# Kernel optimization log

Hardware: AMD Instinct MI355X
Metric: run time of the kernel (lower is better)

The kernel has to match this reference:

```python
import jax, jax.numpy as jnp
import numpy as np

B, T, I, Hd = 64, 1024, 256, 256
SIGMA = 0.01


def setup_inputs() -> dict:
    key = jax.random.key(0)
    ks = jax.random.split(key, 7)
    return {
        "inputs": jax.random.normal(ks[0], (B, T, I), dtype=jnp.float32),
        "W_xz": jax.random.normal(ks[1], (I, Hd), dtype=jnp.float32) * SIGMA,
        "W_hz": jax.random.normal(ks[2], (Hd, Hd), dtype=jnp.float32) * SIGMA,
        "b_z": jnp.zeros((Hd,), dtype=jnp.float32),
        "W_xr": jax.random.normal(ks[3], (I, Hd), dtype=jnp.float32) * SIGMA,
        "W_hr": jax.random.normal(ks[4], (Hd, Hd), dtype=jnp.float32) * SIGMA,
        "b_r": jnp.zeros((Hd,), dtype=jnp.float32),
        "W_xh": jax.random.normal(ks[5], (I, Hd), dtype=jnp.float32) * SIGMA,
        "W_hh": jax.random.normal(ks[6], (Hd, Hd), dtype=jnp.float32) * SIGMA,
        "b_h": jnp.zeros((Hd,), dtype=jnp.float32),
    }


def reference(inputs, W_xz, W_hz, b_z, W_xr, W_hr, b_r, W_xh, W_hh, b_h):
    # inputs: [B, T, I] -> time-major [T, B, I]
    xs = jnp.swapaxes(inputs, 0, 1)
    # Precompute all input-side projections in three big GEMMs (same math,
    # hoisted out of the recurrence): [T, B, Hd] each.
    xz = jnp.einsum("tbi,ih->tbh", xs, W_xz) + b_z
    xr = jnp.einsum("tbi,ih->tbh", xs, W_xr) + b_r
    xh = jnp.einsum("tbi,ih->tbh", xs, W_xh) + b_h

    H0 = jnp.zeros((inputs.shape[0], W_hz.shape[0]), dtype=inputs.dtype)

    def step(H, x):
        xz_t, xr_t, xh_t = x
        Z = jax.nn.sigmoid(xz_t + H @ W_hz)
        R = jax.nn.sigmoid(xr_t + H @ W_hr)
        H_tilde = jnp.tanh(xh_t + (R * H) @ W_hh)
        H_new = Z * H + (1.0 - Z) * H_tilde
        return H_new, H_new

    H_last, outs = jax.lax.scan(step, H0, (xz, xr, xh))
    # outputs stacked along dim=1: [B, T, Hd]
    outputs = jnp.swapaxes(outs, 0, 1)
    return outputs, H_last
```

## Files before the change

### kernel.cpp

```cpp
#include <hip/hip_runtime.h>
#include <math.h>

#define BB 64
#define TT 1024
#define II 256
#define HD 256

typedef unsigned short ushort_t;
typedef unsigned int uint_t;

typedef short sh8 __attribute__((ext_vector_type(8)));
typedef float fx4 __attribute__((ext_vector_type(4)));

__device__ __forceinline__ ushort_t f2bf(float f) {
    uint_t u = __float_as_uint(f);
    uint_t r = (u + 0x7fffu + ((u >> 16) & 1u)) >> 16;
    return (ushort_t)r;
}
__device__ __forceinline__ float bf2f(ushort_t v) {
    return __uint_as_float(((uint_t)v) << 16);
}

__device__ __forceinline__ float fast_rcp(float x) {
#if __has_builtin(__builtin_amdgcn_rcpf)
    return __builtin_amdgcn_rcpf(x);
#else
    return 1.f / x;
#endif
}
__device__ __forceinline__ float sigm(float x) {
    return fast_rcp(1.f + __expf(-x));
}
__device__ __forceinline__ float tanh_fast(float x) {
    return 1.f - 2.f * fast_rcp(1.f + __expf(2.f * x));
}

__device__ __forceinline__ fx4 mfma16(sh8 a, sh8 b, fx4 c) {
    return __builtin_amdgcn_mfma_f32_16x16x32_bf16(a, b, c, 0, 0, 0);
}

__device__ __forceinline__ void async_g2l(const ushort_t* g, ushort_t* l) {
#if __has_builtin(__builtin_amdgcn_global_load_lds)
    __builtin_amdgcn_global_load_lds(
        (const __attribute__((address_space(1))) unsigned int*)g,
        (__attribute__((address_space(3))) unsigned int*)l, 16, 0, 0);
#else
    *reinterpret_cast<uint4*>(l) = *reinterpret_cast<const uint4*>(g);
#endif
}

#define BAR() asm volatile("s_waitcnt lgkmcnt(0)\n\ts_barrier" ::: "memory")

__global__ __launch_bounds__(256) void prepack_kernel(
    const float* __restrict__ Wz, const float* __restrict__ Wr,
    const float* __restrict__ Wh,
    ushort_t* __restrict__ Tz, ushort_t* __restrict__ Tr,
    ushort_t* __restrict__ Th)
{
    const int idx = blockIdx.x * 256 + threadIdx.x;
    const int j = idx >> 8;
    const int k = idx & 255;
    const float* W = (blockIdx.y == 0) ? Wz : (blockIdx.y == 1) ? Wr : Wh;
    ushort_t* T = (blockIdx.y == 0) ? Tz : (blockIdx.y == 1) ? Tr : Th;
    T[idx] = f2bf(W[k * HD + j]);
}

__global__ __launch_bounds__(256) void proj_kernel(
    const float* __restrict__ X,
    const float* __restrict__ Wz, const float* __restrict__ Wr,
    const float* __restrict__ Wh,
    const float* __restrict__ bz, const float* __restrict__ br,
    const float* __restrict__ bh,
    ushort_t* __restrict__ x5)
{
    __shared__ float As[64][36];
    __shared__ float Bs[32][64];
    __shared__ ushort_t ep[8 * 8 * 64];

    const int tid  = threadIdx.x;
    const int tx   = tid & 15;
    const int ty   = tid >> 4;
    const int bg8  = blockIdx.x >> 7;
    const int t0   = (blockIdx.x & 127) * 8;
    const int g    = blockIdx.y >> 2;
    const int col0 = (blockIdx.y & 3) * 64;

    const float* W    = (g == 0) ? Wz : (g == 1) ? Wr : Wh;
    const float* bias = (g == 0) ? bz : (g == 1) ? br : bh;

    float acc[4][4];
#pragma unroll
    for (int i = 0; i < 4; ++i)
#pragma unroll
        for (int j = 0; j < 4; ++j) acc[i][j] = 0.f;

    for (int k0 = 0; k0 < II; k0 += 32) {
        int fi = tid;
#pragma unroll
        for (int rp = 0; rp < 2; ++rp, fi += 256) {
            const int row = fi >> 3;
            const int fc  = fi & 7;
            const size_t m = (size_t)(bg8 * 8 + (row >> 3)) * 1024 + t0 + (row & 7);
            const float4 v = *reinterpret_cast<const float4*>(
                X + m * II + k0 + fc * 4);
            *reinterpret_cast<float4*>(&As[row][fc * 4]) = v;
        }
        fi = tid;
#pragma unroll
        for (int rp = 0; rp < 2; ++rp, fi += 256) {
            const int row = fi >> 4;
            const int fc  = fi & 15;
            const float4 v = *reinterpret_cast<const float4*>(
                W + (size_t)(k0 + row) * HD + col0 + fc * 4);
            *reinterpret_cast<float4*>(&Bs[row][fc * 4]) = v;
        }
        __syncthreads();

#pragma unroll
        for (int kk = 0; kk < 32; ++kk) {
            const float a0 = As[ty * 4 + 0][kk];
            const float a1 = As[ty * 4 + 1][kk];
            const float a2 = As[ty * 4 + 2][kk];
            const float a3 = As[ty * 4 + 3][kk];
            const float4 bv = *reinterpret_cast<const float4*>(&Bs[kk][tx * 4]);
            acc[0][0] += a0 * bv.x; acc[0][1] += a0 * bv.y;
            acc[0][2] += a0 * bv.z; acc[0][3] += a0 * bv.w;
            acc[1][0] += a1 * bv.x; acc[1][1] += a1 * bv.y;
            acc[1][2] += a1 * bv.z; acc[1][3] += a1 * bv.w;
            acc[2][0] += a2 * bv.x; acc[2][1] += a2 * bv.y;
            acc[2][2] += a2 * bv.z; acc[2][3] += a2 * bv.w;
            acc[3][0] += a3 * bv.x; acc[3][1] += a3 * bv.y;
            acc[3][2] += a3 * bv.z; acc[3][3] += a3 * bv.w;
        }
        __syncthreads();
    }

    const float4 bia = *reinterpret_cast<const float4*>(bias + col0 + tx * 4);
#pragma unroll
    for (int i = 0; i < 4; ++i) {
        const int rr = ty * 4 + i;
        const int bi = rr >> 3;
        const int ti = rr & 7;
        ep[ti * 512 + bi * 64 + tx * 4 + 0] = f2bf(acc[i][0] + bia.x);
        ep[ti * 512 + bi * 64 + tx * 4 + 1] = f2bf(acc[i][1] + bia.y);
        ep[ti * 512 + bi * 64 + tx * 4 + 2] = f2bf(acc[i][2] + bia.z);
        ep[ti * 512 + bi * 64 + tx * 4 + 3] = f2bf(acc[i][3] + bia.w);
    }
    __syncthreads();

    const uint4* eps = (const uint4*)ep;
#pragma unroll
    for (int it = 0; it < 2; ++it) {
        const int idx  = it * 256 + tid;
        const int ti   = idx >> 6;
        const int bi   = (idx >> 3) & 7;
        const int part = idx & 7;
        ushort_t* dst = x5 +
            (((size_t)(t0 + ti) * 64 + (bg8 * 8 + bi)) * 3 + g) * 256 +
            col0 + part * 8;
        *reinterpret_cast<uint4*>(dst) = eps[idx];
    }
}

#define XB_U16 768

__global__ __launch_bounds__(512, 2) void gru_recur(
    const ushort_t* __restrict__ x5,
    const ushort_t* __restrict__ Tz, const ushort_t* __restrict__ Tr,
    const ushort_t* __restrict__ Th,
    float* __restrict__ out)
{
    __shared__ __align__(16) ushort_t Hl[264];
    __shared__ __align__(16) ushort_t Rl[264];
    __shared__ __align__(16) ushort_t Xb[2][XB_U16];

    const int tid  = threadIdx.x;
    const int lane = tid & 63;
    const int w    = tid >> 6;
    const int kq   = lane >> 4;
    const int ml   = lane & 15;
    const int cl   = lane & 31;
    const int gate = lane >> 5;
    const int sel  = (lane >> 4) & 1;
    const int j    = w * 32 + cl;
    const int b    = blockIdx.x;

    sh8 wz[2][8], wr[2][8], wh[2][8];
#pragma unroll
    for (int cc = 0; cc < 2; ++cc) {
        const int jw = w * 32 + cc * 16 + ml;
        const size_t rb = (size_t)jw * 256 + kq * 8;
#pragma unroll
        for (int kt = 0; kt < 8; ++kt) {
            wz[cc][kt] = *reinterpret_cast<const sh8*>(Tz + rb + kt * 32);
            wr[cc][kt] = *reinterpret_cast<const sh8*>(Tr + rb + kt * 32);
            wh[cc][kt] = *reinterpret_cast<const sh8*>(Th + rb + kt * 32);
        }
    }

    if (tid < 132) { ((uint_t*)Hl)[tid] = 0u; ((uint_t*)Rl)[tid] = 0u; }

    float hk = 0.f;

    if (tid < 96) async_g2l(x5 + (size_t)b * XB_U16 + tid * 8, &Xb[0][tid * 8]);
    asm volatile("s_waitcnt vmcnt(0)" ::: "memory");
    __syncthreads();

    const ushort_t* harow = Hl + kq * 8;
    const ushort_t* rarow = Rl + kq * 8;
    float* ob = out + (size_t)b * TT * HD;

    const fx4 zero4 = {0.f, 0.f, 0.f, 0.f};
    int cur = 0;
    for (int t = 0; t < TT; ++t) {
        {
            const int tn = (t < TT - 1) ? t + 1 : t;
            if (tid < 96)
                async_g2l(x5 + ((size_t)tn * 64 + b) * XB_U16 + tid * 8,
                          &Xb[cur ^ 1][tid * 8]);
        }
        const ushort_t* xc = Xb[cur];

        fx4 az0 = zero4, az1 = zero4, ar0 = zero4, ar1 = zero4;
#pragma unroll
        for (int kt = 0; kt < 8; ++kt) {
            const sh8 a = *reinterpret_cast<const sh8*>(harow + kt * 32);
            az0 = mfma16(a, wz[0][kt], az0);
            az1 = mfma16(a, wz[1][kt], az1);
            ar0 = mfma16(a, wr[0][kt], ar0);
            ar1 = mfma16(a, wr[1][kt], ar1);
        }
        const float v0 = gate ? ar0[0] : az0[0];
        const float v1 = gate ? ar1[0] : az1[0];
        const float v  = sel ? v1 : v0;
        const float xg = bf2f(xc[gate * 256 + j]);
        const float s  = sigm(xg + v);
        const float zreg = s;
        const float hsh  = __shfl(hk, cl);
        if (gate) Rl[j] = f2bf(s * hsh);
        BAR();

        fx4 ah0 = zero4, ah1 = zero4;
#pragma unroll
        for (int kt = 0; kt < 8; ++kt) {
            const sh8 a = *reinterpret_cast<const sh8*>(rarow + kt * 32);
            ah0 = mfma16(a, wh[0][kt], ah0);
            ah1 = mfma16(a, wh[1][kt], ah1);
        }
        float hn = hk;
        if (!gate) {
            const float va = sel ? ah1[0] : ah0[0];
            const float xh = bf2f(xc[512 + j]);
            const float th = tanh_fast(xh + va);
            hn = zreg * hk + (1.f - zreg) * th;
            hk = hn;
            Hl[j] = f2bf(hn);
        }
        asm volatile("s_waitcnt vmcnt(0)" ::: "memory");
        BAR();

        if (!gate) ob[(size_t)t * HD + j] = hn;
        cur ^= 1;
    }

    if (!gate) out[(size_t)BB * TT * HD + (size_t)b * HD + j] = hk;
}

extern "C" void kernel_launch(void* const* d_in, const int* in_sizes, int n_in,
                              void* d_out, int out_size, void* d_ws, size_t ws_size,
                              hipStream_t stream) {
    const float* X   = (const float*)d_in[0];
    const float* Wxz = (const float*)d_in[1];
    const float* Whz = (const float*)d_in[2];
    const float* bz  = (const float*)d_in[3];
    const float* Wxr = (const float*)d_in[4];
    const float* Whr = (const float*)d_in[5];
    const float* br  = (const float*)d_in[6];
    const float* Wxh = (const float*)d_in[7];
    const float* Whh = (const float*)d_in[8];
    const float* bh  = (const float*)d_in[9];
    float* out = (float*)d_out;

    const size_t X5_BYTES = (size_t)TT * BB * 3 * 256 * 2;
    ushort_t* x5 = (ushort_t*)d_ws;
    ushort_t* Tz = (ushort_t*)((char*)d_ws + X5_BYTES);
    ushort_t* Tr = Tz + HD * HD;
    ushort_t* Th = Tr + HD * HD;

    prepack_kernel<<<dim3(256, 3), 256, 0, stream>>>(Whz, Whr, Whh, Tz, Tr, Th);
    proj_kernel<<<dim3(1024, 12), 256, 0, stream>>>(X, Wxz, Wxr, Wxh, bz, br, bh, x5);
    gru_recur<<<dim3(64), 512, 0, stream>>>(x5, Tz, Tr, Th, out);
}
```

Baseline: 1.560 ms.

## Move input projection to split-bf16 MFMA and reorder recurrence loads

Replaces the scalar fp32 SIMT input-projection GEMM with an MFMA kernel. It splits activations and weights into bf16 hi/lo parts and uses three MFMAs per tile to keep near-fp32 accuracy, with the prepack kernel now producing the hi/lo weight tiles. The recurrence kernel hoists the x-gate loads and shuffle ahead of the MFMA chain and splits the candidate-gate accumulation into two independent chains. Its launch bound also drops to one block per SM. The cost targeted is the projection GEMM, though the recurrence is likely the dominant, latency-bound part.

```diff
diff --git a/kernel.cpp b/kernel.cpp
--- a/kernel.cpp
+++ b/kernel.cpp
@@ -11,6 +11,7 @@
 
 typedef short sh8 __attribute__((ext_vector_type(8)));
 typedef float fx4 __attribute__((ext_vector_type(4)));
+typedef uint_t u32x4 __attribute__((ext_vector_type(4)));
 
 __device__ __forceinline__ ushort_t f2bf(float f) {
     uint_t u = __float_as_uint(f);
@@ -37,6 +38,15 @@
 
 __device__ __forceinline__ fx4 mfma16(sh8 a, sh8 b, fx4 c) {
     return __builtin_amdgcn_mfma_f32_16x16x32_bf16(a, b, c, 0, 0, 0);
+}
+
+__device__ __forceinline__ void split2(float a, float b, uint_t& hi, uint_t& lo) {
+    const uint_t ua = __float_as_uint(a), ub = __float_as_uint(b);
+    hi = (ua >> 16) | (ub & 0xffff0000u);
+    const float la = a - __uint_as_float(ua & 0xffff0000u);
+    const float lb = b - __uint_as_float(ub & 0xffff0000u);
+    const uint_t ula = __float_as_uint(la), ulb = __float_as_uint(lb);
+    lo = (ula >> 16) | (ulb & 0xffff0000u);
 }
 
 __device__ __forceinline__ void async_g2l(const ushort_t* g, ushort_t* l) {
@@ -54,117 +64,120 @@
 __global__ __launch_bounds__(256) void prepack_kernel(
     const float* __restrict__ Wz, const float* __restrict__ Wr,
     const float* __restrict__ Wh,
+    const float* __restrict__ Xz, const float* __restrict__ Xr,
+    const float* __restrict__ Xh,
     ushort_t* __restrict__ Tz, ushort_t* __restrict__ Tr,
-    ushort_t* __restrict__ Th)
+    ushort_t* __restrict__ Th,
+    ushort_t* __restrict__ Thi, ushort_t* __restrict__ Tlo)
 {
     const int idx = blockIdx.x * 256 + threadIdx.x;
     const int j = idx >> 8;
     const int k = idx & 255;
-    const float* W = (blockIdx.y == 0) ? Wz : (blockIdx.y == 1) ? Wr : Wh;
-    ushort_t* T = (blockIdx.y == 0) ? Tz : (blockIdx.y == 1) ? Tr : Th;
-    T[idx] = f2bf(W[k * HD + j]);
-}
-
-__global__ __launch_bounds__(256) void proj_kernel(
+    const int y = blockIdx.y;
+    if (y < 3) {
+        const float* W = (y == 0) ? Wz : (y == 1) ? Wr : Wh;
+        ushort_t* T = (y == 0) ? Tz : (y == 1) ? Tr : Th;
+        T[idx] = f2bf(W[k * HD + j]);
+    } else {
+        const int g = y - 3;
+        const float* W = (g == 0) ? Xz : (g == 1) ? Xr : Xh;
+        const float wv = W[k * HD + j];
+        const ushort_t hi = f2bf(wv);
+        Thi[g * 65536 + idx] = hi;
+        Tlo[g * 65536 + idx] = f2bf(wv - bf2f(hi));
+    }
+}
+
+__global__ __launch_bounds__(256) void proj_mfma(
     const float* __restrict__ X,
-    const float* __restrict__ Wz, const float* __restrict__ Wr,
-    const float* __restrict__ Wh,
+    const ushort_t* __restrict__ Thi, const ushort_t* __restrict__ Tlo,
     const float* __restrict__ bz, const float* __restrict__ br,
     const float* __restrict__ bh,
     ushort_t* __restrict__ x5)
 {
-    __shared__ float As[64][36];
-    __shared__ float Bs[32][64];
-    __shared__ ushort_t ep[8 * 8 * 64];
+    __shared__ __align__(16) ushort_t ep[64 * 256];
 
     const int tid  = threadIdx.x;
-    const int tx   = tid & 15;
-    const int ty   = tid >> 4;
-    const int bg8  = blockIdx.x >> 7;
-    const int t0   = (blockIdx.x & 127) * 8;
-    const int g    = blockIdx.y >> 2;
-    const int col0 = (blockIdx.y & 3) * 64;
-
-    const float* W    = (g == 0) ? Wz : (g == 1) ? Wr : Wh;
+    const int lane = tid & 63;
+    const int w    = tid >> 6;
+    const int kq   = lane >> 4;
+    const int ml   = lane & 15;
+    const int m0   = blockIdx.x * 64;
+    const int g    = blockIdx.y;
+
+    const ushort_t* Bh = Thi + (size_t)g * 65536;
+    const ushort_t* Bl = Tlo + (size_t)g * 65536;
     const float* bias = (g == 0) ? bz : (g == 1) ? br : bh;
 
-    float acc[4][4];
-#pragma unroll
-    for (int i = 0; i < 4; ++i)
-#pragma unroll
-        for (int j = 0; j < 4; ++j) acc[i][j] = 0.f;
-
-    for (int k0 = 0; k0 < II; k0 += 32) {
-        int fi = tid;
-#pragma unroll
-        for (int rp = 0; rp < 2; ++rp, fi += 256) {
-            const int row = fi >> 3;
-            const int fc  = fi & 7;
-            const size_t m = (size_t)(bg8 * 8 + (row >> 3)) * 1024 + t0 + (row & 7);
-            const float4 v = *reinterpret_cast<const float4*>(
-                X + m * II + k0 + fc * 4);
-            *reinterpret_cast<float4*>(&As[row][fc * 4]) = v;
-        }
-        fi = tid;
-#pragma unroll
-        for (int rp = 0; rp < 2; ++rp, fi += 256) {
-            const int row = fi >> 4;
-            const int fc  = fi & 15;
-            const float4 v = *reinterpret_cast<const float4*>(
-                W + (size_t)(k0 + row) * HD + col0 + fc * 4);
-            *reinterpret_cast<float4*>(&Bs[row][fc * 4]) = v;
-        }
-        __syncthreads();
-
-#pragma unroll
-        for (int kk = 0; kk < 32; ++kk) {
-            const float a0 = As[ty * 4 + 0][kk];
-            const float a1 = As[ty * 4 + 1][kk];
-            const float a2 = As[ty * 4 + 2][kk];
-            const float a3 = As[ty * 4 + 3][kk];
-            const float4 bv = *reinterpret_cast<const float4*>(&Bs[kk][tx * 4]);
-            acc[0][0] += a0 * bv.x; acc[0][1] += a0 * bv.y;
-            acc[0][2] += a0 * bv.z; acc[0][3] += a0 * bv.w;
-            acc[1][0] += a1 * bv.x; acc[1][1] += a1 * bv.y;
-            acc[1][2] += a1 * bv.z; acc[1][3] += a1 * bv.w;
-            acc[2][0] += a2 * bv.x; acc[2][1] += a2 * bv.y;
-            acc[2][2] += a2 * bv.z; acc[2][3] += a2 * bv.w;
-            acc[3][0] += a3 * bv.x; acc[3][1] += a3 * bv.y;
-            acc[3][2] += a3 * bv.z; acc[3][3] += a3 * bv.w;
-        }
-        __syncthreads();
-    }
-
-    const float4 bia = *reinterpret_cast<const float4*>(bias + col0 + tx * 4);
-#pragma unroll
-    for (int i = 0; i < 4; ++i) {
-        const int rr = ty * 4 + i;
-        const int bi = rr >> 3;
-        const int ti = rr & 7;
-        ep[ti * 512 + bi * 64 + tx * 4 + 0] = f2bf(acc[i][0] + bia.x);
-        ep[ti * 512 + bi * 64 + tx * 4 + 1] = f2bf(acc[i][1] + bia.y);
-        ep[ti * 512 + bi * 64 + tx * 4 + 2] = f2bf(acc[i][2] + bia.z);
-        ep[ti * 512 + bi * 64 + tx * 4 + 3] = f2bf(acc[i][3] + bia.w);
+    const fx4 zero4 = {0.f, 0.f, 0.f, 0.f};
+    fx4 acc[4][4];
+#pragma unroll
+    for (int mt = 0; mt < 4; ++mt)
+#pragma unroll
+        for (int nt = 0; nt < 4; ++nt) acc[mt][nt] = zero4;
+
+    for (int kt = 0; kt < 8; ++kt) {
+        const int koff = kq * 8 + kt * 32;
+        sh8 bhi[4], blo[4];
+#pragma unroll
+        for (int nt = 0; nt < 4; ++nt) {
+            const size_t rb = (size_t)(w * 64 + nt * 16 + ml) * 256 + koff;
+            bhi[nt] = *reinterpret_cast<const sh8*>(Bh + rb);
+            blo[nt] = *reinterpret_cast<const sh8*>(Bl + rb);
+        }
+#pragma unroll
+        for (int mt = 0; mt < 4; ++mt) {
+            const float* xp = X + (size_t)(m0 + mt * 16 + ml) * II + koff;
+            const float4 f0 = *reinterpret_cast<const float4*>(xp);
+            const float4 f1 = *reinterpret_cast<const float4*>(xp + 4);
+            uint_t hv0, hv1, hv2, hv3, lv0, lv1, lv2, lv3;
+            split2(f0.x, f0.y, hv0, lv0);
+            split2(f0.z, f0.w, hv1, lv1);
+            split2(f1.x, f1.y, hv2, lv2);
+            split2(f1.z, f1.w, hv3, lv3);
+            const u32x4 hq = {hv0, hv1, hv2, hv3};
+            const u32x4 lq = {lv0, lv1, lv2, lv3};
+            const sh8 ahi = __builtin_bit_cast(sh8, hq);
+            const sh8 alo = __builtin_bit_cast(sh8, lq);
+#pragma unroll
+            for (int nt = 0; nt < 4; ++nt) {
+                acc[mt][nt] = mfma16(ahi, bhi[nt], acc[mt][nt]);
+                acc[mt][nt] = mfma16(alo, bhi[nt], acc[mt][nt]);
+                acc[mt][nt] = mfma16(ahi, blo[nt], acc[mt][nt]);
+            }
+        }
+    }
+
+#pragma unroll
+    for (int nt = 0; nt < 4; ++nt) {
+        const int col = w * 64 + nt * 16 + ml;
+        const float bv = bias[col];
+#pragma unroll
+        for (int mt = 0; mt < 4; ++mt)
+#pragma unroll
+            for (int r = 0; r < 4; ++r)
+                ep[(mt * 16 + kq * 4 + r) * 256 + col] =
+                    f2bf(acc[mt][nt][r] + bv);
     }
     __syncthreads();
 
-    const uint4* eps = (const uint4*)ep;
-#pragma unroll
-    for (int it = 0; it < 2; ++it) {
+    const int b   = m0 >> 10;
+    const int t0m = m0 & 1023;
+    const uint4* eps = reinterpret_cast<const uint4*>(ep);
+#pragma unroll
+    for (int it = 0; it < 8; ++it) {
         const int idx  = it * 256 + tid;
-        const int ti   = idx >> 6;
-        const int bi   = (idx >> 3) & 7;
-        const int part = idx & 7;
-        ushort_t* dst = x5 +
-            (((size_t)(t0 + ti) * 64 + (bg8 * 8 + bi)) * 3 + g) * 256 +
-            col0 + part * 8;
-        *reinterpret_cast<uint4*>(dst) = eps[idx];
+        const int rr   = idx >> 5;
+        const int part = idx & 31;
+        uint4* dst = reinterpret_cast<uint4*>(
+            x5 + ((size_t)(t0m + rr) * 64 + b) * 768 + g * 256) + part;
+        *dst = eps[idx];
     }
 }
 
 #define XB_U16 768
 
-__global__ __launch_bounds__(512, 2) void gru_recur(
+__global__ __launch_bounds__(512, 1) void gru_recur(
     const ushort_t* __restrict__ x5,
     const ushort_t* __restrict__ Tz, const ushort_t* __restrict__ Tr,
     const ushort_t* __restrict__ Th,
@@ -221,6 +234,10 @@
         }
         const ushort_t* xc = Xb[cur];
 
+        const float hsh  = __shfl(hk, cl);
+        const float xg   = bf2f(xc[gate * 256 + j]);
+        const float xh_r = bf2f(xc[512 + j]);
+
         fx4 az0 = zero4, az1 = zero4, ar0 = zero4, ar1 = zero4;
 #pragma unroll
         for (int kt = 0; kt < 8; ++kt) {
@@ -233,25 +250,25 @@
         const float v0 = gate ? ar0[0] : az0[0];
         const float v1 = gate ? ar1[0] : az1[0];
         const float v  = sel ? v1 : v0;
-        const float xg = bf2f(xc[gate * 256 + j]);
         const float s  = sigm(xg + v);
         const float zreg = s;
-        const float hsh  = __shfl(hk, cl);
         if (gate) Rl[j] = f2bf(s * hsh);
         BAR();
 
-        fx4 ah0 = zero4, ah1 = zero4;
-#pragma unroll
-        for (int kt = 0; kt < 8; ++kt) {
-            const sh8 a = *reinterpret_cast<const sh8*>(rarow + kt * 32);
-            ah0 = mfma16(a, wh[0][kt], ah0);
-            ah1 = mfma16(a, wh[1][kt], ah1);
+        fx4 ah0a = zero4, ah0b = zero4, ah1a = zero4, ah1b = zero4;
+#pragma unroll
+        for (int kt = 0; kt < 8; kt += 2) {
+            const sh8 a0 = *reinterpret_cast<const sh8*>(rarow + kt * 32);
+            const sh8 a1 = *reinterpret_cast<const sh8*>(rarow + (kt + 1) * 32);
+            ah0a = mfma16(a0, wh[0][kt], ah0a);
+            ah1a = mfma16(a0, wh[1][kt], ah1a);
+            ah0b = mfma16(a1, wh[0][kt + 1], ah0b);
+            ah1b = mfma16(a1, wh[1][kt + 1], ah1b);
         }
         float hn = hk;
         if (!gate) {
-            const float va = sel ? ah1[0] : ah0[0];
-            const float xh = bf2f(xc[512 + j]);
-            const float th = tanh_fast(xh + va);
+            const float va = sel ? (ah1a[0] + ah1b[0]) : (ah0a[0] + ah0b[0]);
+            const float th = tanh_fast(xh_r + va);
             hn = zreg * hk + (1.f - zreg) * th;
             hk = hn;
             Hl[j] = f2bf(hn);
@@ -282,12 +299,16 @@
     float* out = (float*)d_out;
 
     const size_t X5_BYTES = (size_t)TT * BB * 3 * 256 * 2;
-    ushort_t* x5 = (ushort_t*)d_ws;
-    ushort_t* Tz = (ushort_t*)((char*)d_ws + X5_BYTES);
-    ushort_t* Tr = Tz + HD * HD;
-    ushort_t* Th = Tr + HD * HD;
-
-    prepack_kernel<<<dim3(256, 3), 256, 0, stream>>>(Whz, Whr, Whh, Tz, Tr, Th);
-    proj_kernel<<<dim3(1024, 12), 256, 0, stream>>>(X, Wxz, Wxr, Wxh, bz, br, bh, x5);
+    ushort_t* x5  = (ushort_t*)d_ws;
+    ushort_t* Tz  = (ushort_t*)((char*)d_ws + X5_BYTES);
+    ushort_t* Tr  = Tz + HD * HD;
+    ushort_t* Th  = Tr + HD * HD;
+    ushort_t* Thi = Th + HD * HD;
+    ushort_t* Tlo = Thi + 3 * HD * HD;
+
+    prepack_kernel<<<dim3(256, 6), 256, 0, stream>>>(
+        Whz, Whr, Whh, Wxz, Wxr, Wxh, Tz, Tr, Th, Thi, Tlo);
+    proj_mfma<<<dim3(1024, 3), 256, 0, stream>>>(
+        X, Thi, Tlo, bz, br, bh, x5);
     gru_recur<<<dim3(64), 512, 0, stream>>>(x5, Tz, Tr, Th, out);
 }
```

New measurement: 1.412 ms. 1.1x faster.
